# Optimization experiments

Hardware: AMD Instinct MI355X
Metric: run time of the kernel (lower is better)

## Reference

```python
import jax, jax.numpy as jnp
import numpy as np

K = 9  # kernel_size (knn neighbors, loop=True -> self included)

def setup_inputs() -> dict:
    key = jax.random.key(0)
    k1, k2, k3 = jax.random.split(key, 3)
    B, C, H, W = 8, 64, 32, 32
    OUT = 64
    x = jax.random.normal(k1, (B, C, H, W), dtype=jnp.float32)
    # SAGEConv params: lin_l (neighbor aggregate, with bias), lin_r (root, no bias)
    s = 1.0 / np.sqrt(C)
    W_l = jax.random.uniform(k2, (OUT, C), minval=-s, maxval=s, dtype=jnp.float32)
    b_l = jnp.zeros((OUT,), dtype=jnp.float32)
    W_r = jax.random.uniform(k3, (OUT, C), minval=-s, maxval=s, dtype=jnp.float32)
    return {"x": x, "W_l": W_l, "b_l": b_l, "W_r": W_r}

def _knn_mean(x_f, batches):
    # squared-euclidean pairwise distances [N, N], masked across batches
    sq = jnp.sum(x_f * x_f, axis=-1)
    dist = sq[:, None] + sq[None, :] - 2.0 * (x_f @ x_f.T)
    cross = batches[:, None] != batches[None, :]
    dist = jnp.where(cross, jnp.inf, dist)
    neg, idx = jax.lax.top_k(-dist, K)          # k nearest (self included, dist 0)
    valid = (neg != -jnp.inf).astype(x_f.dtype)  # handle degenerate last-batch node
    nbr = x_f[idx] * valid[..., None]            # [N, K, C]
    return nbr.sum(axis=1) / valid.sum(axis=1, keepdims=True)

def reference(x, W_l, b_l, W_r):
    B, C, H, Wd = x.shape
    N = B * H * Wd
    x_f = x.transpose(0, 2, 3, 1).reshape(N, C)  # flat_nodes: [B*H*W, C]
    # torch.linspace(0, B, steps=N).to(int64): truncation of i*B/(N-1)
    batches = jnp.linspace(0.0, float(B), N).astype(jnp.int32)
    mean_nbr = _knn_mean(x_f, batches)
    # SAGEConv: lin_l(mean_j x_j) + lin_r(x_i)
    return mean_nbr @ W_l.T + b_l + x_f @ W_r.T
```

## Files before the change

kernel.cpp:

```cpp
#include <hip/hip_runtime.h>
#include <cstdint>
#include <cstddef>


__global__ __launch_bounds__(256) void k_transpose_sq(const float* __restrict__ x,
                                                      float* __restrict__ xf,
                                                      float* __restrict__ sq) {
  __shared__ float tile[64][65];
  int blk = blockIdx.x;
  int b = blk >> 4;
  int hw0 = (blk & 15) << 6;
  int t = threadIdx.x;
  int lane_hw = t & 63;
  int c_base = t >> 6;
#pragma unroll
  for (int i = 0; i < 16; ++i) {
    int c = c_base + (i << 2);
    tile[c][lane_hw] = x[((b * 64 + c) << 10) + hw0 + lane_hw];
  }
  __syncthreads();
  int c_out = t & 63;
  int hw_base = t >> 6;
#pragma unroll
  for (int i = 0; i < 16; ++i) {
    int hw = hw_base + (i << 2);
    xf[(size_t)(((b << 10) + hw0 + hw) << 6) + c_out] = tile[c_out][hw];
  }
  if (t < 64) {
    float s = 0.f;
#pragma unroll
    for (int c = 0; c < 64; ++c) { float v = tile[c][t]; s += v * v; }
    sq[(b << 10) + hw0 + t] = s;
  }
}

__global__ __launch_bounds__(256) void k_dist(const float* __restrict__ xf,
                                              const float* __restrict__ sq,
                                              float* __restrict__ D) {
  __shared__ float As[32][132];
  __shared__ float Bs[32][132];
  int i0 = blockIdx.y << 7;
  int jj0 = blockIdx.x << 7;
  int s = (i0 >= 7168) ? 7168 : (i0 & ~1023);
  int j0 = s + jj0;
  int t = threadIdx.x;
  int tx = t & 15, ty = t >> 4;

  float acc[8][8];
#pragma unroll
  for (int r = 0; r < 8; ++r)
#pragma unroll
    for (int c = 0; c < 8; ++c) acc[r][c] = 0.f;

  for (int pass = 0; pass < 2; ++pass) {
    __syncthreads();
#pragma unroll
    for (int i = 0; i < 4; ++i) {
      int lin = t + (i << 8);
      int m = lin >> 3;
      int k4 = lin & 7;
      const float4 va = *(const float4*)&xf[(size_t)((i0 + m) << 6) + (pass << 5) + (k4 << 2)];
      As[(k4 << 2) + 0][m] = va.x;
      As[(k4 << 2) + 1][m] = va.y;
      As[(k4 << 2) + 2][m] = va.z;
      As[(k4 << 2) + 3][m] = va.w;
      const float4 vb = *(const float4*)&xf[(size_t)((j0 + m) << 6) + (pass << 5) + (k4 << 2)];
      Bs[(k4 << 2) + 0][m] = vb.x;
      Bs[(k4 << 2) + 1][m] = vb.y;
      Bs[(k4 << 2) + 2][m] = vb.z;
      Bs[(k4 << 2) + 3][m] = vb.w;
    }
    __syncthreads();
#pragma unroll 4
    for (int k = 0; k < 32; ++k) {
      float4 a0 = *(const float4*)&As[k][ty << 2];
      float4 a1 = *(const float4*)&As[k][64 + (ty << 2)];
      float4 b0 = *(const float4*)&Bs[k][tx << 2];
      float4 b1 = *(const float4*)&Bs[k][64 + (tx << 2)];
      float av[8] = {a0.x, a0.y, a0.z, a0.w, a1.x, a1.y, a1.z, a1.w};
      float bv[8] = {b0.x, b0.y, b0.z, b0.w, b1.x, b1.y, b1.z, b1.w};
#pragma unroll
      for (int r = 0; r < 8; ++r)
#pragma unroll
        for (int c = 0; c < 8; ++c)
          acc[r][c] += av[r] * bv[c];
    }
  }

  int mrow[8], ncol[8];
#pragma unroll
  for (int r = 0; r < 4; ++r) { mrow[r] = (ty << 2) + r; mrow[4 + r] = 64 + (ty << 2) + r; }
#pragma unroll
  for (int c = 0; c < 4; ++c) { ncol[c] = (tx << 2) + c; ncol[4 + c] = 64 + (tx << 2) + c; }
  float sqi[8], sqj[8];
#pragma unroll
  for (int r = 0; r < 8; ++r) sqi[r] = sq[i0 + mrow[r]];
#pragma unroll
  for (int c = 0; c < 8; ++c) sqj[c] = sq[j0 + ncol[c]];
#pragma unroll
  for (int r = 0; r < 8; ++r) {
    int row = i0 + mrow[r];
    float4 o0, o1;
    o0.x = sqi[r] + sqj[0] - 2.f * acc[r][0];
    o0.y = sqi[r] + sqj[1] - 2.f * acc[r][1];
    o0.z = sqi[r] + sqj[2] - 2.f * acc[r][2];
    o0.w = sqi[r] + sqj[3] - 2.f * acc[r][3];
    o1.x = sqi[r] + sqj[4] - 2.f * acc[r][4];
    o1.y = sqi[r] + sqj[5] - 2.f * acc[r][5];
    o1.z = sqi[r] + sqj[6] - 2.f * acc[r][6];
    o1.w = sqi[r] + sqj[7] - 2.f * acc[r][7];
    *(float4*)&D[((size_t)row << 10) + jj0 + (tx << 2)] = o0;
    *(float4*)&D[((size_t)row << 10) + jj0 + 64 + (tx << 2)] = o1;
  }
}

__global__ __launch_bounds__(256) void k_select(const float* __restrict__ D,
                                                int* __restrict__ idxO) {
  int t = threadIdx.x;
  int lane = t & 63;
  int i = (blockIdx.x << 2) + (t >> 6);
  if (i == 8191) {
    if (lane == 0) idxO[i * 9] = 8191;
    return;
  }
  int s = (i >= 7168) ? 7168 : (i & ~1023);
  bool mlast = (i >= 7168);
  const float* drow = D + ((size_t)i << 10);
  unsigned long long cand[16];
#pragma unroll
  for (int q = 0; q < 16; ++q) {
    int jj = lane + (q << 6);
    float d = drow[jj];
    unsigned u = __float_as_uint(d);
    u = (u & 0x80000000u) ? ~u : (u | 0x80000000u);
    unsigned long long key = ((unsigned long long)u << 32) | (unsigned)jj;
    if (mlast && jj == 1023) key = ~0ull;
    cand[q] = key;
  }
#pragma unroll
  for (int kk = 0; kk < 9; ++kk) {
    unsigned long long m = cand[0];
#pragma unroll
    for (int q = 1; q < 16; ++q) m = (cand[q] < m) ? cand[q] : m;
#pragma unroll
    for (int off = 32; off > 0; off >>= 1) {
      unsigned hi = __shfl_xor((unsigned)(m >> 32), off, 64);
      unsigned lo = __shfl_xor((unsigned)(m & 0xffffffffu), off, 64);
      unsigned long long o = ((unsigned long long)hi << 32) | lo;
      m = (o < m) ? o : m;
    }
    if (lane == 0) idxO[i * 9 + kk] = s + (int)(m & 0xffffffffu);
#pragma unroll
    for (int q = 0; q < 16; ++q) if (cand[q] == m) cand[q] = ~0ull;
  }
}

__global__ __launch_bounds__(256) void k_out(const float* __restrict__ xf,
                                             const int* __restrict__ idxO,
                                             const float* __restrict__ Wl,
                                             const float* __restrict__ bl,
                                             const float* __restrict__ Wr,
                                             float* __restrict__ out) {
  __shared__ float WsL[64][65];
  __shared__ float WsR[64][65];
  int t = threadIdx.x;
#pragma unroll
  for (int i = 0; i < 16; ++i) {
    int lin = t + (i << 8);
    WsL[lin >> 6][lin & 63] = Wl[lin];
    WsR[lin >> 6][lin & 63] = Wr[lin];
  }
  __syncthreads();
  int lane = t & 63;
  float wl[64], wr[64];
#pragma unroll
  for (int c = 0; c < 64; ++c) { wl[c] = WsL[lane][c]; wr[c] = WsR[lane][c]; }
  float bias = bl[lane];
  int wave = t >> 6;
  int n0 = (blockIdx.x << 4) + (wave << 2);
  for (int nn = 0; nn < 4; ++nn) {
    int n = n0 + nn;
    int cnt = (n == 8191) ? 1 : 9;
    float msum = 0.f;
    for (int k = 0; k < cnt; ++k) {
      int j = idxO[n * 9 + k];
      msum += xf[((size_t)j << 6) + lane];
    }
    float mean = msum / (float)cnt;
    float xr = xf[((size_t)n << 6) + lane];
    float acc = bias;
#pragma unroll
    for (int c = 0; c < 64; ++c) {
      float mc = __int_as_float(__builtin_amdgcn_readlane(__float_as_int(mean), c));
      float xc = __int_as_float(__builtin_amdgcn_readlane(__float_as_int(xr), c));
      acc += mc * wl[c];
      acc += xc * wr[c];
    }
    out[((size_t)n << 6) + lane] = acc;
  }
}

extern "C" void kernel_launch(void* const* d_in, const int* in_sizes, int n_in,
                              void* d_out, int out_size, void* d_ws, size_t ws_size,
                              hipStream_t stream) {
  const float* x  = (const float*)d_in[0];
  const float* Wl = (const float*)d_in[1];
  const float* bl = (const float*)d_in[2];
  const float* Wr = (const float*)d_in[3];
  float* out = (float*)d_out;

  char* ws = (char*)d_ws;
  float* xf  = (float*)(ws);
  float* sq  = (float*)(ws + 2097152);
  int*   idx = (int*)  (ws + 2097152 + 32768);
  float* D   = (float*)(ws + 2097152 + 32768 + 294912);

  k_transpose_sq<<<128, 256, 0, stream>>>(x, xf, sq);
  k_dist<<<dim3(8, 64), 256, 0, stream>>>(xf, sq, D);
  k_select<<<2048, 256, 0, stream>>>(D, idx);
  k_out<<<512, 256, 0, stream>>>(xf, idx, Wl, bl, Wr, out);
}
```

Before: 126.2 us.

## Restructure distance GEMM smem layout to swizzled row-major float4 tiles

The distance kernel now loads the full 128x64 A and B tiles into shared memory once, stored as float4 along the channel dimension with an XOR swizzle, replacing the two-pass transposed scalar layout. Each thread takes strided rows and columns (ty+16r, tx+16c) and accumulates four channels per float4 pair. This cuts the scalar transposing LDS stores and one barrier pair, and aims to avoid bank conflicts. The cost is scalar, strided global stores of D instead of float4 stores, more shared memory (64KB), and possibly higher register pressure from 16 float4 operands.

New measurement: 128.4 us. About the same (+1.8%).

```diff
diff --git a/kernel.cpp b/kernel.cpp
--- a/kernel.cpp
+++ b/kernel.cpp
@@ -37,8 +37,8 @@
 __global__ __launch_bounds__(256) void k_dist(const float* __restrict__ xf,
                                               const float* __restrict__ sq,
                                               float* __restrict__ D) {
-  __shared__ float As[32][132];
-  __shared__ float Bs[32][132];
+  __shared__ float4 As4[2048];
+  __shared__ float4 Bs4[2048];
   int i0 = blockIdx.y << 7;
   int jj0 = blockIdx.x << 7;
   int s = (i0 >= 7168) ? 7168 : (i0 & ~1023);
@@ -46,71 +46,55 @@
   int t = threadIdx.x;
   int tx = t & 15, ty = t >> 4;
 
+#pragma unroll
+  for (int i = 0; i < 8; ++i) {
+    int u = t + (i << 8);
+    int q = u & 15, m = u >> 4;
+    int dst = (q << 7) | (m ^ (q & 7));
+    As4[dst] = *(const float4*)&xf[((size_t)(i0 + m) << 6) + (q << 2)];
+    Bs4[dst] = *(const float4*)&xf[((size_t)(j0 + m) << 6) + (q << 2)];
+  }
+  __syncthreads();
+
   float acc[8][8];
 #pragma unroll
   for (int r = 0; r < 8; ++r)
 #pragma unroll
     for (int c = 0; c < 8; ++c) acc[r][c] = 0.f;
 
-  for (int pass = 0; pass < 2; ++pass) {
-    __syncthreads();
-#pragma unroll
-    for (int i = 0; i < 4; ++i) {
-      int lin = t + (i << 8);
-      int m = lin >> 3;
-      int k4 = lin & 7;
-      const float4 va = *(const float4*)&xf[(size_t)((i0 + m) << 6) + (pass << 5) + (k4 << 2)];
-      As[(k4 << 2) + 0][m] = va.x;
-      As[(k4 << 2) + 1][m] = va.y;
-      As[(k4 << 2) + 2][m] = va.z;
-      As[(k4 << 2) + 3][m] = va.w;
-      const float4 vb = *(const float4*)&xf[(size_t)((j0 + m) << 6) + (pass << 5) + (k4 << 2)];
-      Bs[(k4 << 2) + 0][m] = vb.x;
-      Bs[(k4 << 2) + 1][m] = vb.y;
-      Bs[(k4 << 2) + 2][m] = vb.z;
-      Bs[(k4 << 2) + 3][m] = vb.w;
-    }
-    __syncthreads();
-#pragma unroll 4
-    for (int k = 0; k < 32; ++k) {
-      float4 a0 = *(const float4*)&As[k][ty << 2];
-      float4 a1 = *(const float4*)&As[k][64 + (ty << 2)];
-      float4 b0 = *(const float4*)&Bs[k][tx << 2];
-      float4 b1 = *(const float4*)&Bs[k][64 + (tx << 2)];
-      float av[8] = {a0.x, a0.y, a0.z, a0.w, a1.x, a1.y, a1.z, a1.w};
-      float bv[8] = {b0.x, b0.y, b0.z, b0.w, b1.x, b1.y, b1.z, b1.w};
-#pragma unroll
-      for (int r = 0; r < 8; ++r)
-#pragma unroll
-        for (int c = 0; c < 8; ++c)
-          acc[r][c] += av[r] * bv[c];
-    }
-  }
-
-  int mrow[8], ncol[8];
-#pragma unroll
-  for (int r = 0; r < 4; ++r) { mrow[r] = (ty << 2) + r; mrow[4 + r] = 64 + (ty << 2) + r; }
-#pragma unroll
-  for (int c = 0; c < 4; ++c) { ncol[c] = (tx << 2) + c; ncol[4 + c] = 64 + (tx << 2) + c; }
+#pragma unroll 1
+  for (int q = 0; q < 16; ++q) {
+    int base = q << 7;
+    int sw = q & 7;
+    float4 a[8], b[8];
+#pragma unroll
+    for (int r = 0; r < 8; ++r) a[r] = As4[base | ((ty + (r << 4)) ^ sw)];
+#pragma unroll
+    for (int c = 0; c < 8; ++c) b[c] = Bs4[base | ((tx + (c << 4)) ^ sw)];
+#pragma unroll
+    for (int r = 0; r < 8; ++r)
+#pragma unroll
+      for (int c = 0; c < 8; ++c) {
+        float v = acc[r][c];
+        v = fmaf(a[r].x, b[c].x, v);
+        v = fmaf(a[r].y, b[c].y, v);
+        v = fmaf(a[r].z, b[c].z, v);
+        v = fmaf(a[r].w, b[c].w, v);
+        acc[r][c] = v;
+      }
+  }
+
   float sqi[8], sqj[8];
 #pragma unroll
-  for (int r = 0; r < 8; ++r) sqi[r] = sq[i0 + mrow[r]];
-#pragma unroll
-  for (int c = 0; c < 8; ++c) sqj[c] = sq[j0 + ncol[c]];
+  for (int r = 0; r < 8; ++r) sqi[r] = sq[i0 + ty + (r << 4)];
+#pragma unroll
+  for (int c = 0; c < 8; ++c) sqj[c] = sq[j0 + tx + (c << 4)];
 #pragma unroll
   for (int r = 0; r < 8; ++r) {
-    int row = i0 + mrow[r];
-    float4 o0, o1;
-    o0.x = sqi[r] + sqj[0] - 2.f * acc[r][0];
-    o0.y = sqi[r] + sqj[1] - 2.f * acc[r][1];
-    o0.z = sqi[r] + sqj[2] - 2.f * acc[r][2];
-    o0.w = sqi[r] + sqj[3] - 2.f * acc[r][3];
-    o1.x = sqi[r] + sqj[4] - 2.f * acc[r][4];
-    o1.y = sqi[r] + sqj[5] - 2.f * acc[r][5];
-    o1.z = sqi[r] + sqj[6] - 2.f * acc[r][6];
-    o1.w = sqi[r] + sqj[7] - 2.f * acc[r][7];
-    *(float4*)&D[((size_t)row << 10) + jj0 + (tx << 2)] = o0;
-    *(float4*)&D[((size_t)row << 10) + jj0 + 64 + (tx << 2)] = o1;
+    size_t rowbase = ((size_t)(i0 + ty + (r << 4)) << 10) + jj0 + tx;
+#pragma unroll
+    for (int c = 0; c < 8; ++c)
+      D[rowbase + (c << 4)] = sqi[r] + sqj[c] - 2.f * acc[r][c];
   }
 }
 
```
